# Kernel optimization log

Hardware: AMD Instinct MI355X
Metric: run time of the kernel (lower is better)

## Reference

```python
import jax, jax.numpy as jnp
import numpy as np


def setup_inputs() -> dict:
    key = jax.random.key(0)
    k1, k2, k3 = jax.random.split(key, 3)
    B, C, W, H, K = 8, 3, 512, 512, 13
    Wo, Ho = W - K + 1, H - K + 1
    return {
        "img": jax.random.normal(k1, (B, C, W, H), dtype=jnp.float32),
        "hori": jax.random.normal(k2, (B, K, Wo, Ho), dtype=jnp.float32),
        "vert": jax.random.normal(k3, (B, K, Wo, Ho), dtype=jnp.float32),
        "kernel_size": K,
    }


def reference(img, hori, vert, kernel_size):
    # out[b,c,i,j] = sum_{u,v} img[b,c,i+u,j+v] * vert[b,u,i,j] * hori[b,v,i,j]
    K = kernel_size
    B, C, W, H = img.shape
    Wo, Ho = W - K + 1, H - K + 1
    out = jnp.zeros((B, C, Wo, Ho), img.dtype)
    # Fixed small K x K loop over kernel taps; all pixel/batch dims vectorized.
    for v in range(K):
        h_v = hori[:, v][:, None]  # [B,1,Wo,Ho]
        acc = jnp.zeros((B, C, Wo, Ho), img.dtype)
        for u in range(K):
            acc = acc + img[:, :, u:u + Wo, v:v + Ho] * vert[:, u][:, None]
        out = out + acc * h_v
    return out
```

## Files before the change

kernel.cpp:

```cpp
#include <hip/hip_runtime.h>


#define KK 13
#define NB 8
#define NC 3
#define IW 512
#define IH 512
#define WO 500
#define HO 500

__global__ __launch_bounds__(256) void sepconv_kernel(
    const float* __restrict__ img,
    const float* __restrict__ hori,
    const float* __restrict__ vert,
    float* __restrict__ out)
{
    const int tj = threadIdx.x;
    const int i  = blockIdx.y * 2 + threadIdx.y;
    const int b  = blockIdx.z;
    if (tj >= HO / 4) return;
    const int j0 = tj * 4;

    const size_t khw = (size_t)WO * HO;
    const float* vbase = vert + (size_t)b * KK * khw + (size_t)i * HO + j0;
    const float* hbase = hori + (size_t)b * KK * khw + (size_t)i * HO + j0;

    #pragma unroll 1
    for (int c = 0; c < NC; ++c) {
        const float* ibase = img + (((size_t)(b * NC + c) * IW) + i) * IH + j0;

        float tmp[4][KK];
        #pragma unroll
        for (int jq = 0; jq < 4; ++jq)
            #pragma unroll
            for (int v = 0; v < KK; ++v)
                tmp[jq][v] = 0.0f;

        #pragma unroll
        for (int u = 0; u < KK; ++u) {
            const float* rp = ibase + (size_t)u * IH;
            const float4 r0 = *(const float4*)(rp + 0);
            const float4 r1 = *(const float4*)(rp + 4);
            const float4 r2 = *(const float4*)(rp + 8);
            const float4 r3 = *(const float4*)(rp + 12);
            float row[16];
            row[0]  = r0.x; row[1]  = r0.y; row[2]  = r0.z; row[3]  = r0.w;
            row[4]  = r1.x; row[5]  = r1.y; row[6]  = r1.z; row[7]  = r1.w;
            row[8]  = r2.x; row[9]  = r2.y; row[10] = r2.z; row[11] = r2.w;
            row[12] = r3.x; row[13] = r3.y; row[14] = r3.z; row[15] = r3.w;

            const float4 vt = *(const float4*)(vbase + (size_t)u * khw);

            #pragma unroll
            for (int v = 0; v < KK; ++v) {
                tmp[0][v] += row[0 + v] * vt.x;
                tmp[1][v] += row[1 + v] * vt.y;
                tmp[2][v] += row[2 + v] * vt.z;
                tmp[3][v] += row[3 + v] * vt.w;
            }
        }

        float4 o = make_float4(0.f, 0.f, 0.f, 0.f);
        #pragma unroll
        for (int v = 0; v < KK; ++v) {
            const float4 hv = *(const float4*)(hbase + (size_t)v * khw);
            o.x += tmp[0][v] * hv.x;
            o.y += tmp[1][v] * hv.y;
            o.z += tmp[2][v] * hv.z;
            o.w += tmp[3][v] * hv.w;
        }

        float* op = out + (((size_t)(b * NC + c) * WO) + i) * HO + j0;
        *(float4*)op = o;
    }
}

extern "C" void kernel_launch(void* const* d_in, const int* in_sizes, int n_in,
                              void* d_out, int out_size, void* d_ws, size_t ws_size,
                              hipStream_t stream) {
    const float* img  = (const float*)d_in[0];
    const float* hori = (const float*)d_in[1];
    const float* vert = (const float*)d_in[2];
    float* out = (float*)d_out;

    dim3 block(128, 2, 1);
    dim3 grid(1, WO / 2, NB);
    hipLaunchKernelGGL(sepconv_kernel, grid, block, 0, stream, img, hori, vert, out);
}
```

Baseline: 302.4 us.

## Parallelize channels across threads and stage vert/hori rows in shared memory

Each block now handles one output row with three thread rows, one per channel, instead of looping over channels serially per thread. The per-pixel vert and hori coefficients for that row are loaded once cooperatively into LDS and shared by all three channels. The aim is to increase parallelism and remove the serial channel loop, at the cost of a __syncthreads and about 52KB of LDS per block, which may limit occupancy.

```diff
diff --git a/kernel.cpp b/kernel.cpp
--- a/kernel.cpp
+++ b/kernel.cpp
@@ -8,71 +8,86 @@
 #define IH 512
 #define WO 500
 #define HO 500
+#define QROW 125
+#define NTHREADS 384
 
-__global__ __launch_bounds__(256) void sepconv_kernel(
+__global__ __launch_bounds__(NTHREADS) void sepconv_kernel(
     const float* __restrict__ img,
     const float* __restrict__ hori,
     const float* __restrict__ vert,
     float* __restrict__ out)
 {
+    __shared__ float4 s_vert[KK * QROW];
+    __shared__ float4 s_hori[KK * QROW];
+
+    const int tid = threadIdx.y * 128 + threadIdx.x;
+    const int i = blockIdx.y;
+    const int b = blockIdx.z;
+
+    const size_t khw = (size_t)WO * HO;
+    const size_t rowstride4 = khw / 4;
+    const float4* vsrc = (const float4*)(vert + (size_t)b * KK * khw + (size_t)i * HO);
+    const float4* hsrc = (const float4*)(hori + (size_t)b * KK * khw + (size_t)i * HO);
+
+    #pragma unroll
+    for (int f = tid; f < KK * QROW; f += NTHREADS) {
+        const int u = f / QROW;
+        const int q = f - u * QROW;
+        s_vert[f] = vsrc[(size_t)u * rowstride4 + q];
+        s_hori[f] = hsrc[(size_t)u * rowstride4 + q];
+    }
+    __syncthreads();
+
     const int tj = threadIdx.x;
-    const int i  = blockIdx.y * 2 + threadIdx.y;
-    const int b  = blockIdx.z;
-    if (tj >= HO / 4) return;
+    const int c  = threadIdx.y;
+    if (tj >= QROW) return;
     const int j0 = tj * 4;
 
-    const size_t khw = (size_t)WO * HO;
-    const float* vbase = vert + (size_t)b * KK * khw + (size_t)i * HO + j0;
-    const float* hbase = hori + (size_t)b * KK * khw + (size_t)i * HO + j0;
+    const float* ibase = img + (((size_t)(b * NC + c) * IW) + i) * IH + j0;
 
-    #pragma unroll 1
-    for (int c = 0; c < NC; ++c) {
-        const float* ibase = img + (((size_t)(b * NC + c) * IW) + i) * IH + j0;
+    float tmp[4][KK];
+    #pragma unroll
+    for (int jq = 0; jq < 4; ++jq)
+        #pragma unroll
+        for (int v = 0; v < KK; ++v)
+            tmp[jq][v] = 0.0f;
 
-        float tmp[4][KK];
-        #pragma unroll
-        for (int jq = 0; jq < 4; ++jq)
-            #pragma unroll
-            for (int v = 0; v < KK; ++v)
-                tmp[jq][v] = 0.0f;
+    #pragma unroll
+    for (int u = 0; u < KK; ++u) {
+        const float* rp = ibase + (size_t)u * IH;
+        const float4 r0 = *(const float4*)(rp + 0);
+        const float4 r1 = *(const float4*)(rp + 4);
+        const float4 r2 = *(const float4*)(rp + 8);
+        const float4 r3 = *(const float4*)(rp + 12);
+        const float4 vt = s_vert[u * QROW + tj];
+
+        float row[16];
+        row[0]  = r0.x; row[1]  = r0.y; row[2]  = r0.z; row[3]  = r0.w;
+        row[4]  = r1.x; row[5]  = r1.y; row[6]  = r1.z; row[7]  = r1.w;
+        row[8]  = r2.x; row[9]  = r2.y; row[10] = r2.z; row[11] = r2.w;
+        row[12] = r3.x; row[13] = r3.y; row[14] = r3.z; row[15] = r3.w;
 
         #pragma unroll
-        for (int u = 0; u < KK; ++u) {
-            const float* rp = ibase + (size_t)u * IH;
-            const float4 r0 = *(const float4*)(rp + 0);
-            const float4 r1 = *(const float4*)(rp + 4);
-            const float4 r2 = *(const float4*)(rp + 8);
-            const float4 r3 = *(const float4*)(rp + 12);
-            float row[16];
-            row[0]  = r0.x; row[1]  = r0.y; row[2]  = r0.z; row[3]  = r0.w;
-            row[4]  = r1.x; row[5]  = r1.y; row[6]  = r1.z; row[7]  = r1.w;
-            row[8]  = r2.x; row[9]  = r2.y; row[10] = r2.z; row[11] = r2.w;
-            row[12] = r3.x; row[13] = r3.y; row[14] = r3.z; row[15] = r3.w;
+        for (int v = 0; v < KK; ++v) {
+            tmp[0][v] += row[0 + v] * vt.x;
+            tmp[1][v] += row[1 + v] * vt.y;
+            tmp[2][v] += row[2 + v] * vt.z;
+            tmp[3][v] += row[3 + v] * vt.w;
+        }
+    }
 
-            const float4 vt = *(const float4*)(vbase + (size_t)u * khw);
+    float4 o = make_float4(0.f, 0.f, 0.f, 0.f);
+    #pragma unroll
+    for (int v = 0; v < KK; ++v) {
+        const float4 hv = s_hori[v * QROW + tj];
+        o.x += tmp[0][v] * hv.x;
+        o.y += tmp[1][v] * hv.y;
+        o.z += tmp[2][v] * hv.z;
+        o.w += tmp[3][v] * hv.w;
+    }
 
-            #pragma unroll
-            for (int v = 0; v < KK; ++v) {
-                tmp[0][v] += row[0 + v] * vt.x;
-                tmp[1][v] += row[1 + v] * vt.y;
-                tmp[2][v] += row[2 + v] * vt.z;
-                tmp[3][v] += row[3 + v] * vt.w;
-            }
-        }
-
-        float4 o = make_float4(0.f, 0.f, 0.f, 0.f);
-        #pragma unroll
-        for (int v = 0; v < KK; ++v) {
-            const float4 hv = *(const float4*)(hbase + (size_t)v * khw);
-            o.x += tmp[0][v] * hv.x;
-            o.y += tmp[1][v] * hv.y;
-            o.z += tmp[2][v] * hv.z;
-            o.w += tmp[3][v] * hv.w;
-        }
-
-        float* op = out + (((size_t)(b * NC + c) * WO) + i) * HO + j0;
-        *(float4*)op = o;
-    }
+    float* op = out + (((size_t)(b * NC + c) * WO) + i) * HO + j0;
+    *(float4*)op = o;
 }
 
 extern "C" void kernel_launch(void* const* d_in, const int* in_sizes, int n_in,
@@ -83,7 +98,7 @@
     const float* vert = (const float*)d_in[2];
     float* out = (float*)d_out;
 
-    dim3 block(128, 2, 1);
-    dim3 grid(1, WO / 2, NB);
+    dim3 block(128, 3, 1);
+    dim3 grid(1, WO, NB);
     hipLaunchKernelGGL(sepconv_kernel, grid, block, 0, stream, img, hori, vert, out);
 }
```

New measurement: 311.0 us. 2.9% more time.
